# Kernel tuning notes

Hardware: AMD Instinct MI355X
Metric: run time of the kernel (lower is better)

The kernel has to match this reference:

```python
import jax, jax.numpy as jnp
import numpy as np

B, T, D, H = 4, 2048, 1024, 16
DH = D // H
SCALE = 1.0 / np.sqrt(DH)


def setup_inputs() -> dict:
    key = jax.random.key(0)
    ks = jax.random.split(key, 8)
    s = 1.0 / np.sqrt(D)  # keep projections well-scaled
    return {
        "query": jax.random.normal(ks[0], (B, T, D), jnp.float32),
        "key": jax.random.normal(ks[1], (B, T, D), jnp.float32),
        "value": jax.random.normal(ks[2], (B, T, D), jnp.float32),
        "Wq": jax.random.normal(ks[3], (D, D), jnp.float32) * s,
        "bq": jnp.zeros((D,), jnp.float32),
        "Wk": jax.random.normal(ks[4], (D, D), jnp.float32) * s,
        "bk": jnp.zeros((D,), jnp.float32),
        "Wv": jax.random.normal(ks[5], (D, D), jnp.float32) * s,
        "bv": jnp.zeros((D,), jnp.float32),
        "Wo": jax.random.normal(ks[6], (D, D), jnp.float32) * s,
        "bo": jnp.zeros((D,), jnp.float32),
    }


def reference(query, key, value, Wq, bq, Wk, bk, Wv, bv, Wo, bo):
    # Linear projections (torch Linear: x @ W.T + b; W here stored as [out,in])
    Q = query @ Wq.T + bq            # [B,T,D]
    K = key @ Wk.T + bk
    V = value @ Wv.T + bv
    # split heads -> [B,H,T,DH]
    Q = Q.reshape(B, T, H, DH).transpose(0, 2, 1, 3)
    K = K.reshape(B, T, H, DH).transpose(0, 2, 1, 3)
    V = V.reshape(B, T, H, DH).transpose(0, 2, 1, 3)
    # scaled dot-product attention (chunking in the original is a memory
    # optimization, not a math change; no mask, eval-mode dropout = identity)
    scores = jnp.einsum("bhqd,bhkd->bhqk", Q, K) * SCALE
    attn = jax.nn.softmax(scores, axis=-1)
    out = jnp.einsum("bhqk,bhkd->bhqd", attn, V)  # [B,H,T,DH]
    out = out.transpose(0, 2, 1, 3).reshape(B, T, D)
    return out @ Wo.T + bo
```

## Files before the change

### kernel.cpp

```cpp
#include <hip/hip_runtime.h>
#include <hip/hip_bf16.h>

typedef __bf16 bf16x8 __attribute__((ext_vector_type(8)));
typedef float f32x4 __attribute__((ext_vector_type(4)));
typedef float f32x16 __attribute__((ext_vector_type(16)));
typedef unsigned int uint;
typedef unsigned short u16;

#define DEV static __device__ __forceinline__

DEV u16 f2bf(float x) {
    uint u = __builtin_bit_cast(uint, x);
    u += 0x7FFFu + ((u >> 16) & 1u);
    return (u16)(u >> 16);
}

DEV uint cvtpk(float lo, float hi) {
    uint r;
    asm("v_cvt_pk_bf16_f32 %0, %1, %2" : "=v"(r) : "v"(lo), "v"(hi));
    return r;
}

DEV void plswap(uint& a, uint& b) {
    asm("v_permlane32_swap_b32 %0, %1" : "+v"(a), "+v"(b));
}

DEV float max3f(float a, float b, float c) {
    float d;
    asm("v_max3_f32 %0, %1, %2, %3" : "=v"(d) : "v"(a), "v"(b), "v"(c));
    return d;
}

DEV float fexp2(float x) { return __builtin_amdgcn_exp2f(x); }

DEV void gload16(const void* g, void* l) {
    __builtin_amdgcn_global_load_lds((const __attribute__((address_space(1))) void*)g,
                                     (__attribute__((address_space(3))) void*)l,
                                     16, 0, 0);
}

DEV uint4 xpose8(uint4 vd, int l) {
    uint w0 = vd.x, w1 = vd.y, w2 = vd.z, w3 = vd.w;
    {
        int lam = (l >> 5) & 1;
        uint s0 = lam ? w0 : w2, s1 = lam ? w1 : w3;
        uint t0 = __shfl_xor(s0, 32), t1 = __shfl_xor(s1, 32);
        if (lam) { w0 = t0; w1 = t1; } else { w2 = t0; w3 = t1; }
    }
    {
        int lam = (l >> 4) & 1;
        uint s0 = lam ? w0 : w1, s1 = lam ? w2 : w3;
        uint t0 = __shfl_xor(s0, 16), t1 = __shfl_xor(s1, 16);
        if (lam) { w0 = t0; w2 = t1; } else { w1 = t0; w3 = t1; }
    }
    {
        int lam = (l >> 3) & 1;
        uint sA = lam ? ((w0 & 0xFFFFu) | (w1 << 16)) : ((w0 >> 16) | (w1 & 0xFFFF0000u));
        uint sB = lam ? ((w2 & 0xFFFFu) | (w3 << 16)) : ((w2 >> 16) | (w3 & 0xFFFF0000u));
        uint tA = __shfl_xor(sA, 8), tB = __shfl_xor(sB, 8);
        if (lam) {
            w0 = (w0 & 0xFFFF0000u) | (tA & 0xFFFFu);
            w1 = (w1 & 0xFFFF0000u) | (tA >> 16);
            w2 = (w2 & 0xFFFF0000u) | (tB & 0xFFFFu);
            w3 = (w3 & 0xFFFF0000u) | (tB >> 16);
        } else {
            w0 = (w0 & 0xFFFFu) | (tA << 16);
            w1 = (w1 & 0xFFFFu) | (tA & 0xFFFF0000u);
            w2 = (w2 & 0xFFFFu) | (tB << 16);
            w3 = (w3 & 0xFFFFu) | (tB & 0xFFFF0000u);
        }
    }
    return make_uint4(w0, w1, w2, w3);
}

__global__ __launch_bounds__(256) void k_wconv(const float* __restrict__ w0,
                                               const float* __restrict__ w1,
                                               const float* __restrict__ w2,
                                               const float* __restrict__ w3,
                                               u16* __restrict__ out) {
    const int which = blockIdx.x >> 9;
    const float* in = which == 0 ? w0 : (which == 1 ? w1 : (which == 2 ? w2 : w3));
    const long i = (blockIdx.x & 511) * 256 + threadIdx.x;
    const float4* p = (const float4*)in + i * 2;
    float4 a = p[0], b = p[1];
    uint4 dv;
    dv.x = cvtpk(a.x, a.y); dv.y = cvtpk(a.z, a.w);
    dv.z = cvtpk(b.x, b.y); dv.w = cvtpk(b.z, b.w);
    ((uint4*)(out + ((long)which << 20)))[i] = dv;
}

__global__ __launch_bounds__(256, 2) void k_gemm_qkv(
    const float* __restrict__ Aq, const float* __restrict__ Ak,
    const float* __restrict__ Av, const u16* __restrict__ Bw,
    const float* __restrict__ b0, const float* __restrict__ b1,
    const float* __restrict__ b2, u16* __restrict__ Cb) {
    constexpr int N = 1024, K = 1024;
    __shared__ u16 lA[128 * 64];
    __shared__ u16 lB[128 * 64];
    const int tid = threadIdx.x;
    const int l = tid & 63, w = tid >> 6;
    const int lr = l & 15, lk = l >> 4;
    const int wr = w >> 1, wc = w & 1;
    const int nbn = N >> 7;
    const int cpx = (int)gridDim.x >> 3;
    const int wg = (blockIdx.x & 7) * cpx + (blockIdx.x >> 3);
    const int bm = wg / nbn, bn = wg % nbn;
    const int seg = bm >> 6;
    const float* Aseg = seg == 0 ? Aq : (seg == 1 ? Ak : Av);
    const u16* Bseg = Bw + ((long)seg << 20);
    const float* bias = seg == 0 ? b0 : (seg == 1 ? b1 : b2);
    const int bml = bm & 63;

    const int arow = tid >> 3;
    const int acol = (tid & 7) * 8;
    int adst[4];
    const float* asrc[4];
#pragma unroll
    for (int t = 0; t < 4; ++t) {
        int row = t * 32 + arow;
        adst[t] = row * 128 + ((acol * 2) ^ ((row & 7) << 4));
        asrc[t] = Aseg + (long)(bml * 128 + row) * K + acol;
    }
    long bbase[4];
    int bdst[4];
#pragma unroll
    for (int t = 0; t < 4; ++t) {
        int p = (t * 256 + tid) * 16;
        int row = p >> 7;
        int src = (p & 127) ^ ((row & 7) << 4);
        bdst[t] = p;
        bbase[t] = (long)(bn * 128 + row) * (K * 2) + src;
    }
    const int swz = (lr & 7) << 4;
    int aoff[4][2], boff[4][2];
#pragma unroll
    for (int m = 0; m < 4; ++m)
#pragma unroll
        for (int kc = 0; kc < 2; ++kc) {
            aoff[m][kc] = (wr * 64 + m * 16 + lr) * 128 + ((kc * 64 + lk * 16) ^ swz);
            boff[m][kc] = (wc * 64 + m * 16 + lr) * 128 + ((kc * 64 + lk * 16) ^ swz);
        }

    f32x4 acc[4][4] = {};
    const char* gB = (const char*)Bseg;
    const char* lAb = (const char*)lA;
    const char* lBb = (const char*)lB;
    for (int kt = 0; kt < K / 64; ++kt) {
        __syncthreads();
#pragma unroll
        for (int t = 0; t < 4; ++t)
            gload16(gB + bbase[t] + kt * 128, (char*)lB + bdst[t]);
        float4 f0[4], f1[4];
#pragma unroll
        for (int t = 0; t < 4; ++t) {
            const float* s = asrc[t] + kt * 64;
            f0[t] = *(const float4*)s;
            f1[t] = *(const float4*)(s + 4);
        }
#pragma unroll
        for (int t = 0; t < 4; ++t) {
            uint4 dv;
            dv.x = cvtpk(f0[t].x, f0[t].y);
            dv.y = cvtpk(f0[t].z, f0[t].w);
            dv.z = cvtpk(f1[t].x, f1[t].y);
            dv.w = cvtpk(f1[t].z, f1[t].w);
            *(uint4*)((char*)lA + adst[t]) = dv;
        }
        __syncthreads();
#pragma unroll
        for (int kc = 0; kc < 2; ++kc) {
            bf16x8 av[4], bv[4];
#pragma unroll
            for (int m = 0; m < 4; ++m) av[m] = *(const bf16x8*)(lAb + aoff[m][kc]);
#pragma unroll
            for (int n = 0; n < 4; ++n) bv[n] = *(const bf16x8*)(lBb + boff[n][kc]);
#pragma unroll
            for (int m = 0; m < 4; ++m)
#pragma unroll
                for (int n = 0; n < 4; ++n)
                    acc[m][n] = __builtin_amdgcn_mfma_f32_16x16x32_bf16(av[m], bv[n], acc[m][n], 0, 0, 0);
        }
    }

    const int row0 = bm * 128 + wr * 64;
    const int col0 = bn * 128 + wc * 64;
    float bval[4];
#pragma unroll
    for (int n = 0; n < 4; ++n) bval[n] = bias[col0 + n * 16 + lr];
#pragma unroll
    for (int m = 0; m < 4; ++m)
#pragma unroll
        for (int j = 0; j < 4; ++j) {
            int row = row0 + m * 16 + lk * 4 + j;
#pragma unroll
            for (int n = 0; n < 4; ++n)
                Cb[(long)row * N + col0 + n * 16 + lr] = f2bf(acc[m][n][j] + bval[n]);
        }
}

__global__ __launch_bounds__(256, 2) void k_gemm_bt(
    const u16* __restrict__ A, const u16* __restrict__ Bw,
    const float* __restrict__ bias, float* __restrict__ Cf,
    int M, int N, int K) {
    __shared__ u16 lA[128 * 64];
    __shared__ u16 lB[128 * 64];
    const int tid = threadIdx.x;
    const int l = tid & 63, w = tid >> 6;
    const int lr = l & 15, lk = l >> 4;
    const int wr = w >> 1, wc = w & 1;
    const int nbn = N >> 7;
    const int cpx = (int)gridDim.x >> 3;
    const int wg = (blockIdx.x & 7) * cpx + (blockIdx.x >> 3);
    const int bm = wg / nbn, bn = wg % nbn;

    long abase[4], bbase[4];
    int ldst[4];
#pragma unroll
    for (int t = 0; t < 4; ++t) {
        int c = t * 256 + tid;
        int p = c * 16;
        int row = p >> 7;
        int inrow = p & 127;
        int src = inrow ^ ((row & 7) << 4);
        ldst[t] = p;
        abase[t] = (long)(bm * 128 + row) * (K * 2) + src;
        bbase[t] = (long)(bn * 128 + row) * (K * 2) + src;
    }
    const int swz = (lr & 7) << 4;
    int aoff[4][2], boff[4][2];
#pragma unroll
    for (int m = 0; m < 4; ++m)
#pragma unroll
        for (int kc = 0; kc < 2; ++kc) {
            aoff[m][kc] = (wr * 64 + m * 16 + lr) * 128 + ((kc * 64 + lk * 16) ^ swz);
            boff[m][kc] = (wc * 64 + m * 16 + lr) * 128 + ((kc * 64 + lk * 16) ^ swz);
        }

    f32x4 acc[4][4] = {};
    const char* gA = (const char*)A;
    const char* gB = (const char*)Bw;
    const char* lAb = (const char*)lA;
    const char* lBb = (const char*)lB;
    const int nkt = K >> 6;
    for (int kt = 0; kt < nkt; ++kt) {
        __syncthreads();
#pragma unroll
        for (int t = 0; t < 4; ++t)
            gload16(gA + abase[t] + kt * 128, (char*)lA + ldst[t]);
#pragma unroll
        for (int t = 0; t < 4; ++t)
            gload16(gB + bbase[t] + kt * 128, (char*)lB + ldst[t]);
        __syncthreads();
#pragma unroll
        for (int kc = 0; kc < 2; ++kc) {
            bf16x8 av[4], bv[4];
#pragma unroll
            for (int m = 0; m < 4; ++m) av[m] = *(const bf16x8*)(lAb + aoff[m][kc]);
#pragma unroll
            for (int n = 0; n < 4; ++n) bv[n] = *(const bf16x8*)(lBb + boff[n][kc]);
#pragma unroll
            for (int m = 0; m < 4; ++m)
#pragma unroll
                for (int n = 0; n < 4; ++n)
                    acc[m][n] = __builtin_amdgcn_mfma_f32_16x16x32_bf16(av[m], bv[n], acc[m][n], 0, 0, 0);
        }
    }

    const int row0 = bm * 128 + wr * 64;
    const int col0 = bn * 128 + wc * 64;
    float bval[4];
#pragma unroll
    for (int n = 0; n < 4; ++n) bval[n] = bias[col0 + n * 16 + lr];
#pragma unroll
    for (int m = 0; m < 4; ++m)
#pragma unroll
        for (int j = 0; j < 4; ++j) {
            int row = row0 + m * 16 + lk * 4 + j;
#pragma unroll
            for (int n = 0; n < 4; ++n)
                Cf[(long)row * N + col0 + n * 16 + lr] = acc[m][n][j] + bval[n];
        }
}

__global__ __launch_bounds__(512, 4) void k_attn3(
    const u16* __restrict__ Qb, const u16* __restrict__ Kb,
    const u16* __restrict__ Vb, u16* __restrict__ Ob) {
    constexpr int T = 2048, D = 1024;
    __shared__ u16 sK[2][64 * 64];
    __shared__ u16 sVT[2][64 * 64];
    const int tid = threadIdx.x;
    const int l = tid & 63, w = tid >> 6;
    const int hi = l >> 5;
    const int q32 = l & 31;
    const int hi16 = hi * 16;
    const int kswz = (q32 & 7) << 4;
    const int sw0 = (q32 & 7) ^ ((q32 >> 3) & 7);
    const int sw1 = sw0 ^ 4;
    const int bid = blockIdx.x;
    const int bh = (bid & 7) * 8 + ((bid >> 3) & 7);
    const int qt = bid >> 6;
    const int b = bh >> 4, h = bh & 15;

    const char* Qg = (const char*)(Qb + (long)b * T * D + h * 64);
    const char* Kg = (const char*)(Kb + (long)b * T * D + h * 64);
    const char* Vg = (const char*)(Vb + (long)b * T * D + h * 64);
    const int q0 = qt * 256 + w * 32;

    bf16x8 qf[4];
#pragma unroll
    for (int c = 0; c < 4; ++c)
        qf[c] = *(const bf16x8*)(Qg + (long)(q0 + q32) * 2048 + c * 32 + hi16);

    const int krow = tid >> 3;
    const int ksrc = ((tid & 7) * 16) ^ ((krow & 7) << 4);
    const int kdst = tid * 16;

    const int vr = l >> 3;
    const int vkv = w * 8 + vr;
    const int vd0 = (l & 7) * 8;
    const int vtd = vd0 + vr;
    const int vtwOff = vtd * 128 + (((w ^ (vtd & 7) ^ ((vtd >> 3) & 7)) & 7) << 4);

    union { u16 s[8]; bf16x8 v; } ones_u;
#pragma unroll
    for (int i = 0; i < 8; ++i) ones_u.s[i] = 0x3F80;
    const bf16x8 onesv = ones_u.v;

    gload16(Kg + (long)krow * 2048 + ksrc, (char*)sK[0] + kdst);
    uint4 vd = *(const uint4*)(Vg + (long)vkv * 2048 + vd0 * 2);
    {
        uint4 t = xpose8(vd, l);
        *(uint4*)((char*)sVT[0] + vtwOff) = t;
    }
    vd = *(const uint4*)(Vg + (long)(64 + vkv) * 2048 + vd0 * 2);
    __syncthreads();

    f32x16 o[2] = {};
    f32x16 lacc = {};
    float m = -1e30f;
    const float k1 = 0.18033688f;
    const float THR = 44.3616f;

    for (int kt = 0; kt < T / 64; ++kt) {
        if (kt < T / 64 - 1)
            gload16(Kg + (long)((kt + 1) * 64 + krow) * 2048 + ksrc,
                    (char*)sK[(kt + 1) & 1] + kdst);

        const char* kbp = (const char*)sK[kt & 1];
        f32x16 st[2] = {};
        __builtin_amdgcn_s_setprio(1);
#pragma unroll
        for (int c = 0; c < 4; ++c) {
            bf16x8 kf = *(const bf16x8*)(kbp + q32 * 128 + ((c * 32 + hi16) ^ kswz));
            st[0] = __builtin_amdgcn_mfma_f32_32x32x16_bf16(kf, qf[c], st[0], 0, 0, 0);
        }
#pragma unroll
        for (int c = 0; c < 4; ++c) {
            bf16x8 kf = *(const bf16x8*)(kbp + (32 + q32) * 128 + ((c * 32 + hi16) ^ kswz));
            st[1] = __builtin_amdgcn_mfma_f32_32x32x16_bf16(kf, qf[c], st[1], 0, 0, 0);
        }
        __builtin_amdgcn_s_setprio(0);

        float t0 = max3f(st[0][0], st[0][1], st[0][2]);
        float t1 = max3f(st[0][3], st[0][4], st[0][5]);
        float t2 = max3f(st[0][6], st[0][7], st[0][8]);
        float t3 = max3f(st[0][9], st[0][10], st[0][11]);
        float t4 = max3f(st[0][12], st[0][13], st[0][14]);
        float t5 = max3f(st[1][0], st[1][1], st[1][2]);
        float t6 = max3f(st[1][3], st[1][4], st[1][5]);
        float t7 = max3f(st[1][6], st[1][7], st[1][8]);
        float t8 = max3f(st[1][9], st[1][10], st[1][11]);
        float t9 = max3f(st[1][12], st[1][13], st[1][14]);
        float u0 = max3f(t0, t1, t2);
        float u1 = max3f(t3, t4, st[0][15]);
        float u2 = max3f(t5, t6, t7);
        float u3 = max3f(t8, t9, st[1][15]);
        float rm = fmaxf(max3f(u0, u1, u2), u3);

        bool defer = __all(rm <= m + THR);
        if (!defer) {
            float rmw = fmaxf(rm, __shfl_xor(rm, 32));
            float mn = fmaxf(m, rmw);
            float aq = fexp2((m - mn) * k1);
            m = mn;
#pragma unroll
            for (int r = 0; r < 16; ++r) {
                int src = (r & 3) + 8 * (r >> 2) + 4 * hi;
                float ar = __shfl(aq, src);
                o[0][r] *= ar;
                o[1][r] *= ar;
                lacc[r] *= ar;
            }
        }
        float mk = m * k1;
#pragma unroll
        for (int n = 0; n < 2; ++n)
#pragma unroll
            for (int r = 0; r < 16; ++r)
                st[n][r] = fexp2(fmaf(st[n][r], k1, -mk));

        if (kt < T / 64 - 1) {
            uint4 t = xpose8(vd, l);
            *(uint4*)((char*)sVT[(kt + 1) & 1] + vtwOff) = t;
            if (kt < T / 64 - 2)
                vd = *(const uint4*)(Vg + (long)((kt + 2) * 64 + vkv) * 2048 + vd0 * 2);
        }

        const char* vbp = (const char*)sVT[kt & 1];
        __builtin_amdgcn_s_setprio(1);
#pragma unroll
        for (int c = 0; c < 4; ++c) {
            const int n = c >> 1, rb = (c & 1) * 8;
            uint A0 = cvtpk(st[n][rb + 0], st[n][rb + 1]);
            uint A1 = cvtpk(st[n][rb + 2], st[n][rb + 3]);
            uint B0 = cvtpk(st[n][rb + 4], st[n][rb + 5]);
            uint B1 = cvtpk(st[n][rb + 6], st[n][rb + 7]);
            plswap(A0, B0);
            plswap(A1, B1);
            union { uint u[4]; bf16x8 v; } pa;
            pa.u[0] = A0; pa.u[1] = A1; pa.u[2] = B0; pa.u[3] = B1;
            int cb = ((c * 2 + hi) & 7) << 4;
            bf16x8 v0 = *(const bf16x8*)(vbp + q32 * 128 + (cb ^ (sw0 << 4)));
            bf16x8 v1 = *(const bf16x8*)(vbp + (32 + q32) * 128 + (cb ^ (sw1 << 4)));
            o[0] = __builtin_amdgcn_mfma_f32_32x32x16_bf16(pa.v, v0, o[0], 0, 0, 0);
            o[1] = __builtin_amdgcn_mfma_f32_32x32x16_bf16(pa.v, v1, o[1], 0, 0, 0);
            lacc  = __builtin_amdgcn_mfma_f32_32x32x16_bf16(pa.v, onesv, lacc, 0, 0, 0);
        }
        __builtin_amdgcn_s_setprio(0);
        __syncthreads();
    }

#pragma unroll
    for (int r = 0; r < 16; ++r) {
        float inv = 1.f / lacc[r];
        int srcq = (r & 3) + 8 * (r >> 2) + 4 * hi;
        int trow = q0 + srcq;
        char* orow = (char*)Ob + ((long)(b * T + trow) * D + h * 64) * 2;
        *(u16*)(orow + q32 * 2) = f2bf(o[0][r] * inv);
        *(u16*)(orow + (32 + q32) * 2) = f2bf(o[1][r] * inv);
    }
}

extern "C" void kernel_launch(void* const* d_in, const int* in_sizes, int n_in,
                              void* d_out, int out_size, void* d_ws, size_t ws_size,
                              hipStream_t stream) {
    const float* q  = (const float*)d_in[0];
    const float* k  = (const float*)d_in[1];
    const float* v  = (const float*)d_in[2];
    const float* Wq = (const float*)d_in[3];
    const float* bq = (const float*)d_in[4];
    const float* Wk = (const float*)d_in[5];
    const float* bk = (const float*)d_in[6];
    const float* Wv = (const float*)d_in[7];
    const float* bv = (const float*)d_in[8];
    const float* Wo = (const float*)d_in[9];
    const float* bo = (const float*)d_in[10];

    const long MT = 8192L * 1024;
    const long WT = 1024L * 1024;
    u16* ws   = (u16*)d_ws;
    u16* wall = ws;
    u16* qbf  = wall + 4 * WT;
    u16* kbf  = qbf + MT;
    u16* vbf  = kbf + MT;
    u16* abf  = vbf + MT;

    k_wconv<<<dim3(2048), dim3(256), 0, stream>>>(Wq, Wk, Wv, Wo, wall);

    k_gemm_qkv<<<dim3(1536), dim3(256), 0, stream>>>(q, k, v, wall,
                                                     bq, bk, bv, qbf);

    k_attn3<<<dim3(512), dim3(512), 0, stream>>>(qbf, kbf, vbf, abf);

    k_gemm_bt<<<dim3(512), dim3(256), 0, stream>>>(abf, wall + 3 * WT, bo,
                                                   (float*)d_out, 8192, 1024, 1024);
}
```

Baseline: 221.0 us.

## Write V transposed from QKV GEMM epilogue and load it directly in attention

The QKV projection epilogue now writes the V segment in a per-head transposed [B,H,DH,T] layout instead of row-major. The attention kernel then stages V tiles with async global-to-LDS loads like K, removing the register-level shuffle transpose and the software-pipelined V register prefetch. The cost is a strided, poorly coalesced 2-byte scatter store in the GEMM epilogue for the V third of the output.

```diff
diff --git a/kernel.cpp b/kernel.cpp
--- a/kernel.cpp
+++ b/kernel.cpp
@@ -37,40 +37,6 @@
     __builtin_amdgcn_global_load_lds((const __attribute__((address_space(1))) void*)g,
                                      (__attribute__((address_space(3))) void*)l,
                                      16, 0, 0);
-}
-
-DEV uint4 xpose8(uint4 vd, int l) {
-    uint w0 = vd.x, w1 = vd.y, w2 = vd.z, w3 = vd.w;
-    {
-        int lam = (l >> 5) & 1;
-        uint s0 = lam ? w0 : w2, s1 = lam ? w1 : w3;
-        uint t0 = __shfl_xor(s0, 32), t1 = __shfl_xor(s1, 32);
-        if (lam) { w0 = t0; w1 = t1; } else { w2 = t0; w3 = t1; }
-    }
-    {
-        int lam = (l >> 4) & 1;
-        uint s0 = lam ? w0 : w1, s1 = lam ? w2 : w3;
-        uint t0 = __shfl_xor(s0, 16), t1 = __shfl_xor(s1, 16);
-        if (lam) { w0 = t0; w2 = t1; } else { w1 = t0; w3 = t1; }
-    }
-    {
-        int lam = (l >> 3) & 1;
-        uint sA = lam ? ((w0 & 0xFFFFu) | (w1 << 16)) : ((w0 >> 16) | (w1 & 0xFFFF0000u));
-        uint sB = lam ? ((w2 & 0xFFFFu) | (w3 << 16)) : ((w2 >> 16) | (w3 & 0xFFFF0000u));
-        uint tA = __shfl_xor(sA, 8), tB = __shfl_xor(sB, 8);
-        if (lam) {
-            w0 = (w0 & 0xFFFF0000u) | (tA & 0xFFFFu);
-            w1 = (w1 & 0xFFFF0000u) | (tA >> 16);
-            w2 = (w2 & 0xFFFF0000u) | (tB & 0xFFFFu);
-            w3 = (w3 & 0xFFFF0000u) | (tB >> 16);
-        } else {
-            w0 = (w0 & 0xFFFFu) | (tA << 16);
-            w1 = (w1 & 0xFFFFu) | (tA & 0xFFFF0000u);
-            w2 = (w2 & 0xFFFFu) | (tB << 16);
-            w3 = (w3 & 0xFFFFu) | (tB & 0xFFFF0000u);
-        }
-    }
-    return make_uint4(w0, w1, w2, w3);
 }
 
 __global__ __launch_bounds__(256) void k_wconv(const float* __restrict__ w0,
@@ -93,7 +59,8 @@
     const float* __restrict__ Aq, const float* __restrict__ Ak,
     const float* __restrict__ Av, const u16* __restrict__ Bw,
     const float* __restrict__ b0, const float* __restrict__ b1,
-    const float* __restrict__ b2, u16* __restrict__ Cb) {
+    const float* __restrict__ b2, u16* __restrict__ Cb,
+    u16* __restrict__ VT) {
     constexpr int N = 1024, K = 1024;
     __shared__ u16 lA[128 * 64];
     __shared__ u16 lB[128 * 64];
@@ -182,20 +149,39 @@
         }
     }
 
-    const int row0 = bm * 128 + wr * 64;
     const int col0 = bn * 128 + wc * 64;
     float bval[4];
 #pragma unroll
     for (int n = 0; n < 4; ++n) bval[n] = bias[col0 + n * 16 + lr];
-#pragma unroll
-    for (int m = 0; m < 4; ++m)
-#pragma unroll
-        for (int j = 0; j < 4; ++j) {
-            int row = row0 + m * 16 + lk * 4 + j;
-#pragma unroll
-            for (int n = 0; n < 4; ++n)
-                Cb[(long)row * N + col0 + n * 16 + lr] = f2bf(acc[m][n][j] + bval[n]);
-        }
+
+    if (seg < 2) {
+        const int row0 = bm * 128 + wr * 64;
+#pragma unroll
+        for (int m = 0; m < 4; ++m)
+#pragma unroll
+            for (int j = 0; j < 4; ++j) {
+                int row = row0 + m * 16 + lk * 4 + j;
+#pragma unroll
+                for (int n = 0; n < 4; ++n)
+                    Cb[(long)row * N + col0 + n * 16 + lr] = f2bf(acc[m][n][j] + bval[n]);
+            }
+    } else {
+        const int r0 = bml * 128 + wr * 64;
+#pragma unroll
+        for (int m = 0; m < 4; ++m)
+#pragma unroll
+            for (int j = 0; j < 4; ++j) {
+                int r8 = r0 + m * 16 + lk * 4 + j;
+                int bb = r8 >> 11, t = r8 & 2047;
+#pragma unroll
+                for (int n = 0; n < 4; ++n) {
+                    int col = col0 + n * 16 + lr;
+                    int hh = col >> 6, dh = col & 63;
+                    VT[(((long)(bb * 16 + hh) * 64 + dh) << 11) + t] =
+                        f2bf(acc[m][n][j] + bval[n]);
+                }
+            }
+    }
 }
 
 __global__ __launch_bounds__(256, 2) void k_gemm_bt(
@@ -282,20 +268,19 @@
         }
 }
 
-__global__ __launch_bounds__(512, 4) void k_attn3(
+__global__ __launch_bounds__(512, 4) void k_attn5(
     const u16* __restrict__ Qb, const u16* __restrict__ Kb,
-    const u16* __restrict__ Vb, u16* __restrict__ Ob) {
+    const u16* __restrict__ VTb, u16* __restrict__ Ob) {
     constexpr int T = 2048, D = 1024;
-    __shared__ u16 sK[2][64 * 64];
-    __shared__ u16 sVT[2][64 * 64];
+    constexpr int NT = T / 64;
+    __shared__ u16 sK[2][4096];
+    __shared__ u16 sV[2][4096];
     const int tid = threadIdx.x;
     const int l = tid & 63, w = tid >> 6;
     const int hi = l >> 5;
     const int q32 = l & 31;
     const int hi16 = hi * 16;
     const int kswz = (q32 & 7) << 4;
-    const int sw0 = (q32 & 7) ^ ((q32 >> 3) & 7);
-    const int sw1 = sw0 ^ 4;
     const int bid = blockIdx.x;
     const int bh = (bid & 7) * 8 + ((bid >> 3) & 7);
     const int qt = bid >> 6;
@@ -303,7 +288,7 @@
 
     const char* Qg = (const char*)(Qb + (long)b * T * D + h * 64);
     const char* Kg = (const char*)(Kb + (long)b * T * D + h * 64);
-    const char* Vg = (const char*)(Vb + (long)b * T * D + h * 64);
+    const char* VTg = (const char*)(VTb + (long)bh * 64 * 2048);
     const int q0 = qt * 256 + w * 32;
 
     bf16x8 qf[4];
@@ -311,28 +296,23 @@
     for (int c = 0; c < 4; ++c)
         qf[c] = *(const bf16x8*)(Qg + (long)(q0 + q32) * 2048 + c * 32 + hi16);
 
-    const int krow = tid >> 3;
-    const int ksrc = ((tid & 7) * 16) ^ ((krow & 7) << 4);
-    const int kdst = tid * 16;
-
-    const int vr = l >> 3;
-    const int vkv = w * 8 + vr;
-    const int vd0 = (l & 7) * 8;
-    const int vtd = vd0 + vr;
-    const int vtwOff = vtd * 128 + (((w ^ (vtd & 7) ^ ((vtd >> 3) & 7)) & 7) << 4);
+    const int srow = tid >> 3;
+    const int ssrc = ((tid & 7) * 16) ^ ((srow & 7) << 4);
+    const int sdst = tid * 16;
+    const long kbase = (long)srow * 2048 + ssrc;
+    const long vbase = (long)srow * 4096 + ssrc;
 
     union { u16 s[8]; bf16x8 v; } ones_u;
 #pragma unroll
     for (int i = 0; i < 8; ++i) ones_u.s[i] = 0x3F80;
     const bf16x8 onesv = ones_u.v;
 
-    gload16(Kg + (long)krow * 2048 + ksrc, (char*)sK[0] + kdst);
-    uint4 vd = *(const uint4*)(Vg + (long)vkv * 2048 + vd0 * 2);
-    {
-        uint4 t = xpose8(vd, l);
-        *(uint4*)((char*)sVT[0] + vtwOff) = t;
-    }
-    vd = *(const uint4*)(Vg + (long)(64 + vkv) * 2048 + vd0 * 2);
+#define STAGE(kt_, buf_) do {                                                  \
+        gload16(Kg + (long)(kt_) * 64 * 2048 + kbase, (char*)sK[buf_] + sdst); \
+        gload16(VTg + (kt_) * 128 + vbase, (char*)sV[buf_] + sdst);            \
+    } while (0)
+
+    STAGE(0, 0);
     __syncthreads();
 
     f32x16 o[2] = {};
@@ -341,10 +321,8 @@
     const float k1 = 0.18033688f;
     const float THR = 44.3616f;
 
-    for (int kt = 0; kt < T / 64; ++kt) {
-        if (kt < T / 64 - 1)
-            gload16(Kg + (long)((kt + 1) * 64 + krow) * 2048 + ksrc,
-                    (char*)sK[(kt + 1) & 1] + kdst);
+    for (int kt = 0; kt < NT; ++kt) {
+        if (kt + 1 < NT) STAGE(kt + 1, (kt + 1) & 1);
 
         const char* kbp = (const char*)sK[kt & 1];
         f32x16 st[2] = {};
@@ -399,14 +377,7 @@
             for (int r = 0; r < 16; ++r)
                 st[n][r] = fexp2(fmaf(st[n][r], k1, -mk));
 
-        if (kt < T / 64 - 1) {
-            uint4 t = xpose8(vd, l);
-            *(uint4*)((char*)sVT[(kt + 1) & 1] + vtwOff) = t;
-            if (kt < T / 64 - 2)
-                vd = *(const uint4*)(Vg + (long)((kt + 2) * 64 + vkv) * 2048 + vd0 * 2);
-        }
-
-        const char* vbp = (const char*)sVT[kt & 1];
+        const char* vbp = (const char*)sV[kt & 1];
         __builtin_amdgcn_s_setprio(1);
 #pragma unroll
         for (int c = 0; c < 4; ++c) {
@@ -419,9 +390,9 @@
             plswap(A1, B1);
             union { uint u[4]; bf16x8 v; } pa;
             pa.u[0] = A0; pa.u[1] = A1; pa.u[2] = B0; pa.u[3] = B1;
-            int cb = ((c * 2 + hi) & 7) << 4;
-            bf16x8 v0 = *(const bf16x8*)(vbp + q32 * 128 + (cb ^ (sw0 << 4)));
-            bf16x8 v1 = *(const bf16x8*)(vbp + (32 + q32) * 128 + (cb ^ (sw1 << 4)));
+            int cb = c * 32 + hi16;
+            bf16x8 v0 = *(const bf16x8*)(vbp + q32 * 128 + (cb ^ kswz));
+            bf16x8 v1 = *(const bf16x8*)(vbp + (32 + q32) * 128 + (cb ^ kswz));
             o[0] = __builtin_amdgcn_mfma_f32_32x32x16_bf16(pa.v, v0, o[0], 0, 0, 0);
             o[1] = __builtin_amdgcn_mfma_f32_32x32x16_bf16(pa.v, v1, o[1], 0, 0, 0);
             lacc  = __builtin_amdgcn_mfma_f32_32x32x16_bf16(pa.v, onesv, lacc, 0, 0, 0);
@@ -429,6 +400,7 @@
         __builtin_amdgcn_s_setprio(0);
         __syncthreads();
     }
+#undef STAGE
 
 #pragma unroll
     for (int r = 0; r < 16; ++r) {
@@ -462,15 +434,15 @@
     u16* wall = ws;
     u16* qbf  = wall + 4 * WT;
     u16* kbf  = qbf + MT;
-    u16* vbf  = kbf + MT;
-    u16* abf  = vbf + MT;
+    u16* vtb  = kbf + MT;
+    u16* abf  = vtb + MT;
 
     k_wconv<<<dim3(2048), dim3(256), 0, stream>>>(Wq, Wk, Wv, Wo, wall);
 
     k_gemm_qkv<<<dim3(1536), dim3(256), 0, stream>>>(q, k, v, wall,
-                                                     bq, bk, bv, qbf);
-
-    k_attn3<<<dim3(512), dim3(512), 0, stream>>>(qbf, kbf, vbf, abf);
+                                                     bq, bk, bv, qbf, vtb);
+
+    k_attn5<<<dim3(512), dim3(512), 0, stream>>>(qbf, kbf, vtb, abf);
 
     k_gemm_bt<<<dim3(512), dim3(256), 0, stream>>>(abf, wall + 3 * WT, bo,
                                                    (float*)d_out, 8192, 1024, 1024);
```

Measured after the change: 191.1 us. 13.5% less time.
